# Kernel optimization log

Measured on AMD Instinct MI355X. Metric: run time of the kernel, lower is better.

## Reference

```python
import jax, jax.numpy as jnp
import numpy as np

K = 16          # knn_graph k
FPS_RATIO = 0.5 # fps ratio
BN_EPS = 1e-5


def knn_idx(p, k):
    # p: [B, N, 3] -> neighbor indices [B, N, k] (loop=True: self included)
    n2 = jnp.sum(p * p, axis=-1)                                  # [B, N]
    d = n2[:, :, None] + n2[:, None, :] - 2.0 * jnp.einsum('bnc,bmc->bnm', p, p)
    _, idx = jax.lax.top_k(-d, k)                                 # smallest distances
    return idx


def gather_nbrs(x, idx):
    # x: [B, N, C], idx: [B, N, k] -> [B, N, k, C]
    return jax.vmap(lambda xb, ib: xb[ib])(x, idx)


def bn_silu(y, g, be):
    # training-mode BatchNorm over all rows (flattened) + SiLU, per PyG MLP defaults
    C = y.shape[-1]
    yf = y.reshape(-1, C)
    mu = jnp.mean(yf, axis=0)
    var = jnp.mean((yf - mu) ** 2, axis=0)
    return jax.nn.silu((y - mu) * jax.lax.rsqrt(var + BN_EPS) * g + be)


def fps_idx(p, m):
    # farthest point sampling on one cloud p: [N, 3], deterministic start at 0
    d0 = jnp.sum((p - p[0]) ** 2, axis=-1)
    def step(mind, _):
        i = jnp.argmax(mind)
        di = jnp.sum((p - p[i]) ** 2, axis=-1)
        return jnp.minimum(mind, di), i.astype(jnp.int32)
    _, idxs = jax.lax.scan(step, d0, None, length=m - 1)
    return jnp.concatenate([jnp.zeros((1,), jnp.int32), idxs])


def setup_inputs() -> dict:
    key = jax.random.key(0)
    ks = jax.random.split(key, 4)
    B, N, zdim = 16, 2048, 256
    return {
        'pos': jax.random.normal(ks[0], (B, N, 3), jnp.float32),
        'W1': jax.random.normal(ks[1], (6, 64), jnp.float32) * (1.0 / np.sqrt(6)),
        'b1': jnp.zeros((64,), jnp.float32),
        'g1': jnp.ones((64,), jnp.float32),
        'be1': jnp.zeros((64,), jnp.float32),
        'W2a': jax.random.normal(ks[2], (67, 128), jnp.float32) * (1.0 / np.sqrt(67)),
        'b2a': jnp.zeros((128,), jnp.float32),
        'g2a': jnp.ones((128,), jnp.float32),
        'be2a': jnp.zeros((128,), jnp.float32),
        'W2b': jax.random.normal(ks[3], (128, zdim), jnp.float32) * (1.0 / np.sqrt(128)),
        'b2b': jnp.zeros((zdim,), jnp.float32),
        'g2b': jnp.ones((zdim,), jnp.float32),
        'be2b': jnp.zeros((zdim,), jnp.float32),
    }


def reference(pos, W1, b1, g1, be1, W2a, b2a, g2a, be2a, W2b, b2b, g2b, be2b):
    B, N, _ = pos.shape
    M = int(N * FPS_RATIO)

    # conv1: knn graph on pos, message = MLP([x_j, pos_j - pos_i]), max-aggr
    idx1 = knn_idx(pos, K)                                  # [B, N, K]
    pos_j = gather_nbrs(pos, idx1)                          # [B, N, K, 3]
    msg = jnp.concatenate([pos_j, pos_j - pos[:, :, None, :]], axis=-1)  # [B,N,K,6]
    h = bn_silu(msg @ W1 + b1, g1, be1)                     # [B, N, K, 64]
    h = jnp.max(h, axis=2)                                  # [B, N, 64]

    # farthest point sampling, ratio 0.5
    idx_f = jax.vmap(fps_idx, in_axes=(0, None))(pos, M)    # [B, M]
    h = jax.vmap(lambda a, i: a[i])(h, idx_f)               # [B, M, 64]
    pos2 = jax.vmap(lambda a, i: a[i])(pos, idx_f)          # [B, M, 3]

    # conv2: knn on sampled points, message = MLP2([h_j, pos_j - pos_i]), max-aggr
    idx2 = knn_idx(pos2, K)                                 # [B, M, K]
    h_j = gather_nbrs(h, idx2)                              # [B, M, K, 64]
    p_j = gather_nbrs(pos2, idx2)                           # [B, M, K, 3]
    msg2 = jnp.concatenate([h_j, p_j - pos2[:, :, None, :]], axis=-1)  # [B,M,K,67]
    h2 = bn_silu(msg2 @ W2a + b2a, g2a, be2a)               # [B, M, K, 128]
    h2 = bn_silu(h2 @ W2b + b2b, g2b, be2b)                 # [B, M, K, zdim]
    h2 = jnp.max(h2, axis=2)                                # [B, M, zdim]

    # global max aggregation per cloud
    return jnp.max(h2, axis=1)                              # [B, zdim]
```

## Files before the change

kernel.cpp:

```cpp
#include <hip/hip_runtime.h>
#include <hip/hip_bf16.h>

#define NB 16
#define NN 2048
#define KNNK 16
#define MM 1024
#define RC1 (NB*NN*KNNK)
#define RC2 (NB*MM*KNNK)

typedef unsigned long long u64;
typedef __attribute__((ext_vector_type(8))) short short8;
typedef __attribute__((ext_vector_type(4))) float f32x4;

__device__ __forceinline__ float frn_mul(float a, float b){ return __fmul_rn(a,b); }
__device__ __forceinline__ float frn_add(float a, float b){ return __fadd_rn(a,b); }
__device__ __forceinline__ float frn_sub(float a, float b){ return __fsub_rn(a,b); }
__device__ __forceinline__ float silu_f(float x){ return x / (1.0f + __expf(-x)); }
__device__ __forceinline__ u64 umax64(u64 a, u64 b){ return a > b ? a : b; }

__device__ __forceinline__ unsigned f32_sortable(float f){
  unsigned u = __float_as_uint(f);
  return u ^ ((unsigned)((int)u >> 31) | 0x80000000u);
}
__device__ __forceinline__ unsigned short f2bf(float f){
  unsigned u = __float_as_uint(f);
  return (unsigned short)((u + 0x7FFFu + ((u >> 16) & 1u)) >> 16);
}
__device__ __forceinline__ float bf2f(unsigned short h){
  return __uint_as_float(((unsigned)h) << 16);
}

__device__ __forceinline__ void atomicMaxF(unsigned* addr, float v){
  if (v >= 0.f) atomicMax((int*)addr, (int)__float_as_uint(v));
  else          atomicMin(addr, __float_as_uint(v));
}
__device__ __forceinline__ void atomicMinF(unsigned* addr, float v){
  if (v >= 0.f) atomicMin((int*)addr, (int)__float_as_uint(v));
  else          atomicMax(addr, __float_as_uint(v));
}

__global__ __launch_bounds__(256) void init_kernel(float* stats1, float* stats2a, float* stats2b,
                                                   unsigned* gmax, unsigned* gmin){
  int t = blockIdx.x*256 + threadIdx.x;
  if (t < 128) stats1[t] = 0.f;
  if (t < 256) stats2a[t] = 0.f;
  if (t < 512) stats2b[t] = 0.f;
  if (t < 4096){ gmax[t] = 0xFF800000u; gmin[t] = 0x7F800000u; }
}

template<int CHUNK>
__device__ __forceinline__ void knn_chunk_body(const float* __restrict__ pos_b, int qbase, int jbase,
                                               float4* sm, u64* __restrict__ out, int tid){
  for (int t = tid; t < CHUNK; t += 256){
    const float* p = pos_b + (size_t)(jbase + t)*3;
    float x = p[0], y = p[1], z = p[2];
    float n2 = frn_add(frn_add(frn_mul(x,x), frn_mul(y,y)), frn_mul(z,z));
    sm[t] = make_float4(x,y,z,n2);
  }
  __syncthreads();
  int i = qbase + tid;
  const float* qp = pos_b + (size_t)i*3;
  float xi = qp[0], yi = qp[1], zi = qp[2];
  float n2i = frn_add(frn_add(frn_mul(xi,xi), frn_mul(yi,yi)), frn_mul(zi,zi));
  u64 best[KNNK];
#pragma unroll
  for (int p = 0; p < KNNK; ++p) best[p] = ~0ull;
  for (int jj = 0; jj < CHUNK; ++jj){
    float4 v = sm[jj];
    float e = frn_add(frn_add(frn_mul(xi,v.x), frn_mul(yi,v.y)), frn_mul(zi,v.z));
    float d = frn_sub(frn_add(n2i, v.w), frn_mul(2.0f, e));
    u64 key = ((u64)f32_sortable(d) << 32) | (unsigned)(jbase + jj);
    if (key < best[KNNK-1]){
      u64 cur = key;
#pragma unroll
      for (int p = 0; p < KNNK; ++p){
        u64 mn = best[p] < cur ? best[p] : cur;
        u64 mx = best[p] < cur ? cur : best[p];
        best[p] = mn; cur = mx;
      }
    }
  }
#pragma unroll
  for (int p = 0; p < KNNK; ++p) out[p] = best[p];
}

__global__ __launch_bounds__(256) void k0_fps_knn1(const float* __restrict__ pos,
    int* __restrict__ idxf, float* __restrict__ pos2, u64* __restrict__ pknn1){
  __shared__ __align__(16) char smem[37*1024];
  int tid = threadIdx.x;
  if (blockIdx.x < 16){
    int b = blockIdx.x;
    float4* pts4 = (float4*)smem;
    int* sel = (int*)(smem + 32*1024);
    u64* wred = (u64*)(smem + 32*1024 + 4096);
    const float* pb = pos + (size_t)b*NN*3;
    float X[8], Y[8], Z[8], MD[8];
    unsigned LO[8];
#pragma unroll
    for (int q = 0; q < 8; ++q){
      int p = tid + 256*q;
      float x = pb[p*3+0], y = pb[p*3+1], z = pb[p*3+2];
      X[q] = x; Y[q] = y; Z[q] = z;
      LO[q] = ~(unsigned)p;
      pts4[p] = make_float4(x, y, z, 0.f);
    }
    float qx = pb[0], qy = pb[1], qz = pb[2];
#pragma unroll
    for (int q = 0; q < 8; ++q){
      float dx = frn_sub(X[q],qx), dy = frn_sub(Y[q],qy), dz = frn_sub(Z[q],qz);
      MD[q] = frn_add(frn_add(frn_mul(dx,dx), frn_mul(dy,dy)), frn_mul(dz,dz));
    }
    if (tid == 0) sel[0] = 0;
    int wv = tid >> 6;
    __syncthreads();
    for (int s = 1; s < MM; ++s){
      u64 t0 = umax64(((u64)__float_as_uint(MD[0])<<32)|LO[0], ((u64)__float_as_uint(MD[1])<<32)|LO[1]);
      u64 t1 = umax64(((u64)__float_as_uint(MD[2])<<32)|LO[2], ((u64)__float_as_uint(MD[3])<<32)|LO[3]);
      u64 t2 = umax64(((u64)__float_as_uint(MD[4])<<32)|LO[4], ((u64)__float_as_uint(MD[5])<<32)|LO[5]);
      u64 t3 = umax64(((u64)__float_as_uint(MD[6])<<32)|LO[6], ((u64)__float_as_uint(MD[7])<<32)|LO[7]);
      u64 kk = umax64(umax64(t0, t1), umax64(t2, t3));
#define RED_DPP(CTRL) { \
      unsigned lo_ = (unsigned)kk, hi_ = (unsigned)(kk>>32); \
      unsigned plo = (unsigned)__builtin_amdgcn_update_dpp((int)lo_,(int)lo_,CTRL,0xF,0xF,false); \
      unsigned phi = (unsigned)__builtin_amdgcn_update_dpp((int)hi_,(int)hi_,CTRL,0xF,0xF,false); \
      u64 o = ((u64)phi<<32)|plo; kk = o > kk ? o : kk; }
      RED_DPP(0xB1)
      RED_DPP(0x4E)
      RED_DPP(0x124)
      RED_DPP(0x128)
      RED_DPP(0x142)
      RED_DPP(0x143)
#undef RED_DPP
      int par = s & 1;
      if ((tid & 63) == 63) wred[par*4 + wv] = kk;
      __syncthreads();
      const u64* wr = wred + par*4;
      u64 K = umax64(umax64(wr[0], wr[1]), umax64(wr[2], wr[3]));
      unsigned wp = ~(unsigned)K;
      if (tid == 0) sel[s] = (int)wp;
      float4 wc = pts4[wp];
#pragma unroll
      for (int q = 0; q < 8; ++q){
        float dx = frn_sub(X[q],wc.x), dy = frn_sub(Y[q],wc.y), dz = frn_sub(Z[q],wc.z);
        float d = frn_add(frn_add(frn_mul(dx,dx), frn_mul(dy,dy)), frn_mul(dz,dz));
        MD[q] = fminf(MD[q], d);
      }
    }
    __syncthreads();
    for (int m = tid; m < MM; m += 256){
      int j = sel[m];
      idxf[b*MM + m] = j;
      float4 c = pts4[j];
      pos2[(size_t)(b*MM+m)*3+0] = c.x;
      pos2[(size_t)(b*MM+m)*3+1] = c.y;
      pos2[(size_t)(b*MM+m)*3+2] = c.z;
    }
  } else {
    int cid = blockIdx.x - 16;
    int b = cid >> 4;
    int rblk = (cid >> 1) & 7;
    int ch = cid & 1;
    float4* sm = (float4*)smem;
    const float* pos_b = pos + (size_t)b*NN*3;
    int i = rblk*256 + tid;
    u64* out = pknn1 + ((size_t)(b*NN + i)*2 + ch)*KNNK;
    knn_chunk_body<1024>(pos_b, rblk*256, ch*1024, sm, out, tid);
  }
}

__global__ __launch_bounds__(256) void k1_merge1_knn2(const u64* __restrict__ pknn1,
    int* __restrict__ idx1, const float* __restrict__ pos2, u64* __restrict__ pknn2){
  __shared__ __align__(16) float4 sm[256];
  int tid = threadIdx.x;
  if (blockIdx.x < 128){
    int row = blockIdx.x*256 + tid;
    const u64* A = pknn1 + (size_t)row*32;
    const u64* B = A + 16;
    int ia = 0, ib = 0;
    int* op = idx1 + (size_t)row*KNNK;
#pragma unroll
    for (int p = 0; p < KNNK; ++p){
      u64 ka = A[ia], kb = B[ib];
      if (ka < kb){ op[p] = (int)(unsigned)ka; ++ia; }
      else        { op[p] = (int)(unsigned)kb; ++ib; }
    }
  } else {
    int cid = blockIdx.x - 128;
    int b = cid >> 4;
    int rblk = (cid >> 2) & 3;
    int ch = cid & 3;
    const float* pos_b = pos2 + (size_t)b*MM*3;
    int i = rblk*256 + tid;
    u64* out = pknn2 + ((size_t)(b*MM + i)*4 + ch)*KNNK;
    knn_chunk_body<256>(pos_b, rblk*256, ch*256, sm, out, tid);
  }
}

__global__ __launch_bounds__(256) void k2_merge2_c1stats(const u64* __restrict__ pknn2,
    int* __restrict__ idx2, const float* __restrict__ pos, const int* __restrict__ idx1,
    const float* __restrict__ W1, const float* __restrict__ b1, float* __restrict__ stats1){
  __shared__ float red[4][64][2];
  int tid = threadIdx.x;
  if (blockIdx.x < 64){
    int row = blockIdx.x*256 + tid;
    const u64* L = pknn2 + (size_t)row*64;
    int o0=0, o1=0, o2=0, o3=0;
    int* op = idx2 + (size_t)row*KNNK;
#pragma unroll
    for (int p = 0; p < KNNK; ++p){
      u64 k0 = L[o0], k1 = L[16+o1], k2 = L[32+o2], k3 = L[48+o3];
      u64 m01 = k0 < k1 ? k0 : k1;
      u64 m23 = k2 < k3 ? k2 : k3;
      u64 m = m01 < m23 ? m01 : m23;
      op[p] = (int)(unsigned)m;
      o0 += (m == k0); o1 += (m == k1); o2 += (m == k2); o3 += (m == k3);
    }
    return;
  }
  int lane = tid & 63, wv = tid >> 6;
  int wave = (blockIdx.x - 64)*4 + wv;
  float w[6];
#pragma unroll
  for (int f = 0; f < 6; ++f) w[f] = W1[f*64 + lane];
  float bias = b1[lane];
  float ssum = 0.f, ssq = 0.f;
  for (int r = 0; r < 8; ++r){
    int row = wave*8 + r;
    int b = row >> 11, ii = row & 2047;
    const float* pi = pos + ((size_t)(b*NN + ii))*3;
    float xi = pi[0], yi = pi[1], zi = pi[2];
    const int* ip = idx1 + (size_t)row * KNNK;
#pragma unroll 4
    for (int k = 0; k < KNNK; ++k){
      int j = ip[k];
      const float* pj = pos + ((size_t)(b*NN + j))*3;
      float xj = pj[0], yj = pj[1], zj = pj[2];
      float y = bias;
      y = fmaf(xj, w[0], y); y = fmaf(yj, w[1], y); y = fmaf(zj, w[2], y);
      y = fmaf(xj - xi, w[3], y); y = fmaf(yj - yi, w[4], y); y = fmaf(zj - zi, w[5], y);
      ssum += y; ssq = fmaf(y, y, ssq);
    }
  }
  red[wv][lane][0] = ssum; red[wv][lane][1] = ssq;
  __syncthreads();
  if (tid < 64){
    float s = red[0][lane][0]+red[1][lane][0]+red[2][lane][0]+red[3][lane][0];
    float q = red[0][lane][1]+red[1][lane][1]+red[2][lane][1]+red[3][lane][1];
    atomicAdd(&stats1[lane], s);
    atomicAdd(&stats1[64+lane], q);
  }
}

__global__ __launch_bounds__(256) void conv1_apply_kernel(
    const float* __restrict__ pos, const int* __restrict__ idx1,
    const float* __restrict__ W1, const float* __restrict__ b1,
    const float* __restrict__ g1, const float* __restrict__ be1,
    const float* __restrict__ stats1, float* __restrict__ h){
  int lane = threadIdx.x & 63, wv = threadIdx.x >> 6;
  int wave = blockIdx.x*4 + wv;
  float w[6];
#pragma unroll
  for (int f = 0; f < 6; ++f) w[f] = W1[f*64 + lane];
  float bias = b1[lane];
  const float inv = 1.0f / (float)RC1;
  float mu = stats1[lane] * inv;
  float var = fmaxf(stats1[64+lane]*inv - mu*mu, 0.f);
  float sc = rsqrtf(var + 1e-5f) * g1[lane];
  float sh = be1[lane] - mu*sc;
  for (int r = 0; r < 8; ++r){
    int row = wave*8 + r;
    int b = row >> 11, ii = row & 2047;
    const float* pi = pos + ((size_t)(b*NN + ii))*3;
    float xi = pi[0], yi = pi[1], zi = pi[2];
    const int* ip = idx1 + (size_t)row * KNNK;
    float ymn = INFINITY, ymx = -INFINITY;
#pragma unroll 4
    for (int k = 0; k < KNNK; ++k){
      int j = ip[k];
      const float* pj = pos + ((size_t)(b*NN + j))*3;
      float xj = pj[0], yj = pj[1], zj = pj[2];
      float y = bias;
      y = fmaf(xj, w[0], y); y = fmaf(yj, w[1], y); y = fmaf(zj, w[2], y);
      y = fmaf(xj - xi, w[3], y); y = fmaf(yj - yi, w[4], y); y = fmaf(zj - zi, w[5], y);
      ymn = fminf(ymn, y); ymx = fmaxf(ymx, y);
    }
    h[((size_t)row << 6) + lane] = fmaxf(silu_f(fmaf(ymx, sc, sh)), silu_f(fmaf(ymn, sc, sh)));
  }
}

__global__ __launch_bounds__(256) void conv2a_kernel(
    const float* __restrict__ h, const int* __restrict__ idxf,
    const float* __restrict__ pos2, const int* __restrict__ idx2,
    const float* __restrict__ W2a, const float* __restrict__ b2a,
    float* __restrict__ stats2a, __hip_bfloat16* __restrict__ y2a){
  __shared__ float Wl[67*128];
  __shared__ float red[4][64][4];
  for (int t = threadIdx.x; t < 67*128; t += 256) Wl[t] = W2a[t];
  __syncthreads();
  int lane = threadIdx.x & 63, wv = threadIdx.x >> 6;
  int wave = blockIdx.x*4 + wv;
  float bias0 = b2a[lane], bias1 = b2a[64+lane];
  float ssum0=0, ssq0=0, ssum1=0, ssq1=0;
  for (int r4 = 0; r4 < 16; ++r4){
    int row0 = wave*64 + r4*4;
    int b = row0 >> 14;
    int m = (row0 >> 4) & 1023;
    int j0 = idx2[row0+0], j1 = idx2[row0+1], j2 = idx2[row0+2], j3 = idx2[row0+3];
    int q0 = idxf[b*MM + j0], q1 = idxf[b*MM + j1], q2 = idxf[b*MM + j2], q3 = idxf[b*MM + j3];
    const float4* h0 = (const float4*)(h + ((size_t)(b*NN + q0) << 6));
    const float4* h1 = (const float4*)(h + ((size_t)(b*NN + q1) << 6));
    const float4* h2 = (const float4*)(h + ((size_t)(b*NN + q2) << 6));
    const float4* h3 = (const float4*)(h + ((size_t)(b*NN + q3) << 6));
    float y00=bias0, y01=bias1, y10=bias0, y11=bias1;
    float y20=bias0, y21=bias1, y30=bias0, y31=bias1;
#define C2A_STEP(e, a0v, a1v, a2v, a3v) { \
      float w0_ = Wl[(e)*128 + lane], w1_ = Wl[(e)*128 + 64 + lane]; \
      y00 = fmaf(a0v, w0_, y00); y01 = fmaf(a0v, w1_, y01); \
      y10 = fmaf(a1v, w0_, y10); y11 = fmaf(a1v, w1_, y11); \
      y20 = fmaf(a2v, w0_, y20); y21 = fmaf(a2v, w1_, y21); \
      y30 = fmaf(a3v, w0_, y30); y31 = fmaf(a3v, w1_, y31); }
#pragma unroll
    for (int f4 = 0; f4 < 16; ++f4){
      float4 v0 = h0[f4], v1 = h1[f4], v2 = h2[f4], v3 = h3[f4];
      C2A_STEP(f4*4+0, v0.x, v1.x, v2.x, v3.x)
      C2A_STEP(f4*4+1, v0.y, v1.y, v2.y, v3.y)
      C2A_STEP(f4*4+2, v0.z, v1.z, v2.z, v3.z)
      C2A_STEP(f4*4+3, v0.w, v1.w, v2.w, v3.w)
    }
    const float* pm = pos2 + ((size_t)(b*MM + m))*3;
    float pmx = pm[0], pmy = pm[1], pmz = pm[2];
    const float* pj0 = pos2 + ((size_t)(b*MM + j0))*3;
    const float* pj1 = pos2 + ((size_t)(b*MM + j1))*3;
    const float* pj2 = pos2 + ((size_t)(b*MM + j2))*3;
    const float* pj3 = pos2 + ((size_t)(b*MM + j3))*3;
    C2A_STEP(64, pj0[0]-pmx, pj1[0]-pmx, pj2[0]-pmx, pj3[0]-pmx)
    C2A_STEP(65, pj0[1]-pmy, pj1[1]-pmy, pj2[1]-pmy, pj3[1]-pmy)
    C2A_STEP(66, pj0[2]-pmz, pj1[2]-pmz, pj2[2]-pmz, pj3[2]-pmz)
#undef C2A_STEP
    ssum0 += y00+y10+y20+y30;
    ssum1 += y01+y11+y21+y31;
    ssq0 = fmaf(y00,y00,fmaf(y10,y10,fmaf(y20,y20,fmaf(y30,y30,ssq0))));
    ssq1 = fmaf(y01,y01,fmaf(y11,y11,fmaf(y21,y21,fmaf(y31,y31,ssq1))));
    y2a[(size_t)(row0+0)*128 + lane]      = __float2bfloat16(y00);
    y2a[(size_t)(row0+0)*128 + 64 + lane] = __float2bfloat16(y01);
    y2a[(size_t)(row0+1)*128 + lane]      = __float2bfloat16(y10);
    y2a[(size_t)(row0+1)*128 + 64 + lane] = __float2bfloat16(y11);
    y2a[(size_t)(row0+2)*128 + lane]      = __float2bfloat16(y20);
    y2a[(size_t)(row0+2)*128 + 64 + lane] = __float2bfloat16(y21);
    y2a[(size_t)(row0+3)*128 + lane]      = __float2bfloat16(y30);
    y2a[(size_t)(row0+3)*128 + 64 + lane] = __float2bfloat16(y31);
  }
  red[wv][lane][0]=ssum0; red[wv][lane][1]=ssq0; red[wv][lane][2]=ssum1; red[wv][lane][3]=ssq1;
  __syncthreads();
  if (threadIdx.x < 64){
    float s0=0,q0=0,s1=0,q1=0;
#pragma unroll
    for (int v2=0; v2<4; ++v2){ s0+=red[v2][lane][0]; q0+=red[v2][lane][1]; s1+=red[v2][lane][2]; q1+=red[v2][lane][3]; }
    atomicAdd(&stats2a[lane], s0);      atomicAdd(&stats2a[128+lane], q0);
    atomicAdd(&stats2a[64+lane], s1);   atomicAdd(&stats2a[192+lane], q1);
  }
}

__global__ __launch_bounds__(256) void conv2b_kernel(
    const __hip_bfloat16* __restrict__ y2a, const float* __restrict__ stats2a,
    const float* __restrict__ g2a, const float* __restrict__ be2a,
    const float* __restrict__ W2b, const float* __restrict__ b2b,
    float* __restrict__ stats2b, unsigned* __restrict__ gmax, unsigned* __restrict__ gmin){
  __shared__ __align__(16) char Albs[64*256];
  __shared__ __align__(16) char Btbs[64*256];
  __shared__ float sc2a[128], sh2a[128];
  int tid = threadIdx.x;
  int lane = tid & 63, wvi = tid >> 6;
  int ct = blockIdx.x & 3;
  int rb = blockIdx.x >> 2;
  int c0 = ct * 64;
  int batch = rb >> 5;
  if (tid < 128){
    const float inv = 1.0f / (float)RC2;
    float mu = stats2a[tid] * inv;
    float var = fmaxf(stats2a[128+tid]*inv - mu*mu, 0.f);
    float s = rsqrtf(var + 1e-5f) * g2a[tid];
    sc2a[tid] = s; sh2a[tid] = be2a[tid] - mu*s;
  }
  {
    int cc = tid & 63, u0 = tid >> 6;
#pragma unroll
    for (int i = 0; i < 4; ++i){
      int u = u0 + i*4;
      unsigned short hb[8];
#pragma unroll
      for (int e = 0; e < 8; ++e) hb[e] = f2bf(W2b[(size_t)(u*8+e)*256 + c0 + cc]);
      *(short8*)(Btbs + cc*256 + u*16) = *(short8*)hb;
    }
  }
  __syncthreads();
  short8 bfrag[4];
#pragma unroll
  for (int kb4 = 0; kb4 < 4; ++kb4){
    int col_local = wvi*16 + (lane & 15);
    bfrag[kb4] = *(short8*)(Btbs + col_local*256 + kb4*64 + (lane>>4)*16);
  }
  float bb = b2b[c0 + wvi*16 + (lane & 15)];
  float vmn = INFINITY, vmx = -INFINITY, ssum = 0.f, ssq = 0.f;
  const unsigned short* y2u = (const unsigned short*)y2a;
  int sr = tid & 63, su = tid >> 6;
  for (int tile = 0; tile < 8; ++tile){
    int row0 = rb*512 + tile*64;
    if (tile > 0) __syncthreads();
#pragma unroll
    for (int i = 0; i < 4; ++i){
      int u = su + i*4;
      short8 v = *(const short8*)(y2u + (size_t)(row0 + sr)*128 + u*8);
      unsigned short ha[8];
#pragma unroll
      for (int e = 0; e < 8; ++e){
        int k = u*8 + e;
        float f = bf2f((unsigned short)v[e]);
        ha[e] = f2bf(silu_f(fmaf(f, sc2a[k], sh2a[k])));
      }
      *(short8*)(Albs + sr*256 + ((u*16) ^ ((sr & 7) << 4))) = *(short8*)ha;
    }
    __syncthreads();
#pragma unroll
    for (int sl = 0; sl < 4; ++sl){
      f32x4 acc = {0.f, 0.f, 0.f, 0.f};
#pragma unroll
      for (int kb4 = 0; kb4 < 4; ++kb4){
        int r = sl*16 + (lane & 15);
        short8 afrag = *(short8*)(Albs + r*256 + ((kb4*64 + (lane>>4)*16) ^ ((r & 7) << 4)));
        acc = __builtin_amdgcn_mfma_f32_16x16x32_bf16(afrag, bfrag[kb4], acc, 0, 0, 0);
      }
#pragma unroll
      for (int j = 0; j < 4; ++j){
        float y = acc[j] + bb;
        vmn = fminf(vmn, y); vmx = fmaxf(vmx, y);
        ssum += y; ssq = fmaf(y, y, ssq);
      }
    }
  }
#pragma unroll
  for (int off = 16; off <= 32; off += 16){
    vmn  = fminf(vmn,  __shfl_xor(vmn,  off));
    vmx  = fmaxf(vmx,  __shfl_xor(vmx,  off));
    ssum = ssum + __shfl_xor(ssum, off);
    ssq  = ssq  + __shfl_xor(ssq,  off);
  }
  if ((lane >> 4) == 0){
    int c = c0 + wvi*16 + lane;
    atomicAdd(&stats2b[c], ssum);
    atomicAdd(&stats2b[256+c], ssq);
    atomicMaxF(&gmax[batch*256 + c], vmx);
    atomicMinF(&gmin[batch*256 + c], vmn);
  }
}

__global__ __launch_bounds__(256) void final_kernel(
    const float* __restrict__ stats2b, const unsigned* __restrict__ gmax,
    const unsigned* __restrict__ gmin, const float* __restrict__ g2b,
    const float* __restrict__ be2b, float* __restrict__ out){
  int t = blockIdx.x*256 + threadIdx.x;
  if (t >= NB*256) return;
  int c = t & 255;
  const float inv = 1.0f / (float)RC2;
  float mu = stats2b[c]*inv;
  float var = fmaxf(stats2b[256+c]*inv - mu*mu, 0.f);
  float sc = rsqrtf(var + 1e-5f)*g2b[c];
  float sh = be2b[c] - mu*sc;
  float mx = __uint_as_float(gmax[t]);
  float mn = __uint_as_float(gmin[t]);
  out[t] = fmaxf(silu_f(fmaf(mx, sc, sh)), silu_f(fmaf(mn, sc, sh)));
}

extern "C" void kernel_launch(void* const* d_in, const int* in_sizes, int n_in,
                              void* d_out, int out_size, void* d_ws, size_t ws_size,
                              hipStream_t stream){
  (void)in_sizes; (void)n_in; (void)out_size; (void)ws_size;
  const float* pos  = (const float*)d_in[0];
  const float* W1   = (const float*)d_in[1];
  const float* b1   = (const float*)d_in[2];
  const float* g1   = (const float*)d_in[3];
  const float* be1  = (const float*)d_in[4];
  const float* W2a  = (const float*)d_in[5];
  const float* b2a  = (const float*)d_in[6];
  const float* g2a  = (const float*)d_in[7];
  const float* be2a = (const float*)d_in[8];
  const float* W2b  = (const float*)d_in[9];
  const float* b2b  = (const float*)d_in[10];
  const float* g2b  = (const float*)d_in[11];
  const float* be2b = (const float*)d_in[12];

  char* w = (char*)d_ws;
  size_t off = 0;
  auto carve = [&](size_t bytes)->void*{ void* p = w + off; off += (bytes + 255) & ~(size_t)255; return p; };
  int*      idx1    = (int*)carve((size_t)NB*NN*KNNK*4);
  float*    h       = (float*)carve((size_t)NB*NN*64*4);
  int*      idxf    = (int*)carve((size_t)NB*MM*4);
  float*    pos2    = (float*)carve((size_t)NB*MM*3*4);
  int*      idx2    = (int*)carve((size_t)NB*MM*KNNK*4);
  float*    stats1  = (float*)carve(128*4);
  float*    stats2a = (float*)carve(256*4);
  float*    stats2b = (float*)carve(512*4);
  unsigned* gmax    = (unsigned*)carve(4096*4);
  unsigned* gmin    = (unsigned*)carve(4096*4);
  __hip_bfloat16* y2a = (__hip_bfloat16*)carve((size_t)RC2*128*2);
  u64* pknn1 = (u64*)y2a;
  u64* pknn2 = (u64*)((char*)y2a + (32u<<20));

  init_kernel<<<dim3(16), dim3(256), 0, stream>>>(stats1, stats2a, stats2b, gmax, gmin);
  k0_fps_knn1<<<dim3(272), dim3(256), 0, stream>>>(pos, idxf, pos2, pknn1);
  k1_merge1_knn2<<<dim3(384), dim3(256), 0, stream>>>(pknn1, idx1, pos2, pknn2);
  k2_merge2_c1stats<<<dim3(1088), dim3(256), 0, stream>>>(pknn2, idx2, pos, idx1, W1, b1, stats1);
  conv1_apply_kernel<<<dim3(1024), dim3(256), 0, stream>>>(pos, idx1, W1, b1, g1, be1, stats1, h);
  conv2a_kernel<<<dim3(1024), dim3(256), 0, stream>>>(h, idxf, pos2, idx2, W2a, b2a, stats2a, y2a);
  conv2b_kernel<<<dim3(2048), dim3(256), 0, stream>>>(y2a, stats2a, g2a, be2a, W2b, b2b, stats2b, gmax, gmin);
  final_kernel<<<dim3(16), dim3(256), 0, stream>>>(stats2b, gmax, gmin, g2b, be2b, (float*)d_out);
}
```

Before: 970.3 us.

## Fuse knn1 with conv1 stats, drop partial-merge passes, merge knn2 with conv1 apply

Each knn1 block now scans all 2048 candidates itself instead of splitting the scan into two chunks, which removes the partial top-k buffers and the merge kernels. The neighbor indices are kept in shared memory and reused for the conv1 BatchNorm statistics in the same block. knn2 is computed without chunking inside the kernel that applies conv1. This cuts the launch count from seven to five and removes the intermediate global traffic, at the cost of fewer, longer knn blocks (128 instead of 256 for knn1, 64 instead of 256 for knn2), which lowers parallelism on a GPU with many CUs.

```diff
diff --git a/kernel.cpp b/kernel.cpp
--- a/kernel.cpp
+++ b/kernel.cpp
@@ -48,51 +48,16 @@
   if (t < 4096){ gmax[t] = 0xFF800000u; gmin[t] = 0x7F800000u; }
 }
 
-template<int CHUNK>
-__device__ __forceinline__ void knn_chunk_body(const float* __restrict__ pos_b, int qbase, int jbase,
-                                               float4* sm, u64* __restrict__ out, int tid){
-  for (int t = tid; t < CHUNK; t += 256){
-    const float* p = pos_b + (size_t)(jbase + t)*3;
-    float x = p[0], y = p[1], z = p[2];
-    float n2 = frn_add(frn_add(frn_mul(x,x), frn_mul(y,y)), frn_mul(z,z));
-    sm[t] = make_float4(x,y,z,n2);
-  }
-  __syncthreads();
-  int i = qbase + tid;
-  const float* qp = pos_b + (size_t)i*3;
-  float xi = qp[0], yi = qp[1], zi = qp[2];
-  float n2i = frn_add(frn_add(frn_mul(xi,xi), frn_mul(yi,yi)), frn_mul(zi,zi));
-  u64 best[KNNK];
-#pragma unroll
-  for (int p = 0; p < KNNK; ++p) best[p] = ~0ull;
-  for (int jj = 0; jj < CHUNK; ++jj){
-    float4 v = sm[jj];
-    float e = frn_add(frn_add(frn_mul(xi,v.x), frn_mul(yi,v.y)), frn_mul(zi,v.z));
-    float d = frn_sub(frn_add(n2i, v.w), frn_mul(2.0f, e));
-    u64 key = ((u64)f32_sortable(d) << 32) | (unsigned)(jbase + jj);
-    if (key < best[KNNK-1]){
-      u64 cur = key;
-#pragma unroll
-      for (int p = 0; p < KNNK; ++p){
-        u64 mn = best[p] < cur ? best[p] : cur;
-        u64 mx = best[p] < cur ? cur : best[p];
-        best[p] = mn; cur = mx;
-      }
-    }
-  }
-#pragma unroll
-  for (int p = 0; p < KNNK; ++p) out[p] = best[p];
-}
-
-__global__ __launch_bounds__(256) void k0_fps_knn1(const float* __restrict__ pos,
-    int* __restrict__ idxf, float* __restrict__ pos2, u64* __restrict__ pknn1){
-  __shared__ __align__(16) char smem[37*1024];
+__global__ __launch_bounds__(256) void k0_mega(const float* __restrict__ pos,
+    int* __restrict__ idxf, float* __restrict__ pos2, int* __restrict__ idx1,
+    const float* __restrict__ W1, const float* __restrict__ b1, float* __restrict__ stats1){
+  __shared__ __align__(16) char smem[51*1024];
   int tid = threadIdx.x;
   if (blockIdx.x < 16){
     int b = blockIdx.x;
     float4* pts4 = (float4*)smem;
     int* sel = (int*)(smem + 32*1024);
-    u64* wred = (u64*)(smem + 32*1024 + 4096);
+    u64* wred = (u64*)(smem + 36*1024);
     const float* pb = pos + (size_t)b*NN*3;
     float X[8], Y[8], Z[8], MD[8];
     unsigned LO[8];
@@ -157,134 +122,149 @@
     }
   } else {
     int cid = blockIdx.x - 16;
-    int b = cid >> 4;
-    int rblk = (cid >> 1) & 7;
-    int ch = cid & 1;
-    float4* sm = (float4*)smem;
-    const float* pos_b = pos + (size_t)b*NN*3;
+    int b = cid >> 3, rblk = cid & 7;
+    float4* pts4 = (float4*)smem;
+    int* idxl = (int*)(smem + 32*1024);
+    float* red = (float*)(smem + 48*1024);
+    const float* pb = pos + (size_t)b*NN*3;
+    for (int i = tid; i < NN; i += 256){
+      float x = pb[i*3+0], y = pb[i*3+1], z = pb[i*3+2];
+      float n2 = frn_add(frn_add(frn_mul(x,x), frn_mul(y,y)), frn_mul(z,z));
+      pts4[i] = make_float4(x, y, z, n2);
+    }
+    __syncthreads();
     int i = rblk*256 + tid;
-    u64* out = pknn1 + ((size_t)(b*NN + i)*2 + ch)*KNNK;
-    knn_chunk_body<1024>(pos_b, rblk*256, ch*1024, sm, out, tid);
-  }
-}
-
-__global__ __launch_bounds__(256) void k1_merge1_knn2(const u64* __restrict__ pknn1,
-    int* __restrict__ idx1, const float* __restrict__ pos2, u64* __restrict__ pknn2){
-  __shared__ __align__(16) float4 sm[256];
-  int tid = threadIdx.x;
-  if (blockIdx.x < 128){
-    int row = blockIdx.x*256 + tid;
-    const u64* A = pknn1 + (size_t)row*32;
-    const u64* B = A + 16;
-    int ia = 0, ib = 0;
-    int* op = idx1 + (size_t)row*KNNK;
+    float4 qv = pts4[i];
+    float xi = qv.x, yi = qv.y, zi = qv.z, n2i = qv.w;
+    u64 best[KNNK];
+#pragma unroll
+    for (int p = 0; p < KNNK; ++p) best[p] = ~0ull;
+    for (int jj = 0; jj < NN; ++jj){
+      float4 v = pts4[jj];
+      float e = frn_add(frn_add(frn_mul(xi,v.x), frn_mul(yi,v.y)), frn_mul(zi,v.z));
+      float d = frn_sub(frn_add(n2i, v.w), frn_mul(2.0f, e));
+      u64 key = ((u64)f32_sortable(d) << 32) | (unsigned)jj;
+      if (key < best[KNNK-1]){
+        u64 cur = key;
+#pragma unroll
+        for (int p = 0; p < KNNK; ++p){
+          u64 mn = best[p] < cur ? best[p] : cur;
+          u64 mx = best[p] < cur ? cur : best[p];
+          best[p] = mn; cur = mx;
+        }
+      }
+    }
+    int* op = idx1 + ((size_t)(b*NN + i))*KNNK;
 #pragma unroll
     for (int p = 0; p < KNNK; ++p){
-      u64 ka = A[ia], kb = B[ib];
-      if (ka < kb){ op[p] = (int)(unsigned)ka; ++ia; }
-      else        { op[p] = (int)(unsigned)kb; ++ib; }
-    }
-  } else {
-    int cid = blockIdx.x - 128;
-    int b = cid >> 4;
-    int rblk = (cid >> 2) & 3;
-    int ch = cid & 3;
-    const float* pos_b = pos2 + (size_t)b*MM*3;
-    int i = rblk*256 + tid;
-    u64* out = pknn2 + ((size_t)(b*MM + i)*4 + ch)*KNNK;
-    knn_chunk_body<256>(pos_b, rblk*256, ch*256, sm, out, tid);
-  }
-}
-
-__global__ __launch_bounds__(256) void k2_merge2_c1stats(const u64* __restrict__ pknn2,
-    int* __restrict__ idx2, const float* __restrict__ pos, const int* __restrict__ idx1,
-    const float* __restrict__ W1, const float* __restrict__ b1, float* __restrict__ stats1){
-  __shared__ float red[4][64][2];
-  int tid = threadIdx.x;
-  if (blockIdx.x < 64){
-    int row = blockIdx.x*256 + tid;
-    const u64* L = pknn2 + (size_t)row*64;
-    int o0=0, o1=0, o2=0, o3=0;
-    int* op = idx2 + (size_t)row*KNNK;
-#pragma unroll
-    for (int p = 0; p < KNNK; ++p){
-      u64 k0 = L[o0], k1 = L[16+o1], k2 = L[32+o2], k3 = L[48+o3];
-      u64 m01 = k0 < k1 ? k0 : k1;
-      u64 m23 = k2 < k3 ? k2 : k3;
-      u64 m = m01 < m23 ? m01 : m23;
-      op[p] = (int)(unsigned)m;
-      o0 += (m == k0); o1 += (m == k1); o2 += (m == k2); o3 += (m == k3);
-    }
-    return;
-  }
-  int lane = tid & 63, wv = tid >> 6;
-  int wave = (blockIdx.x - 64)*4 + wv;
-  float w[6];
-#pragma unroll
-  for (int f = 0; f < 6; ++f) w[f] = W1[f*64 + lane];
-  float bias = b1[lane];
-  float ssum = 0.f, ssq = 0.f;
-  for (int r = 0; r < 8; ++r){
-    int row = wave*8 + r;
-    int b = row >> 11, ii = row & 2047;
-    const float* pi = pos + ((size_t)(b*NN + ii))*3;
-    float xi = pi[0], yi = pi[1], zi = pi[2];
-    const int* ip = idx1 + (size_t)row * KNNK;
+      int j = (int)(unsigned)(best[p] & 0xFFFFFFFFull);
+      op[p] = j;
+      idxl[tid*KNNK + p] = j;
+    }
+    __syncthreads();
+    int lane = tid & 63, wv = tid >> 6;
+    float w[6];
+#pragma unroll
+    for (int f = 0; f < 6; ++f) w[f] = W1[f*64 + lane];
+    float bias = b1[lane];
+    float ssum = 0.f, ssq = 0.f;
+    for (int r = 0; r < 64; ++r){
+      int lrow = wv*64 + r;
+      float4 pi = pts4[rblk*256 + lrow];
+      const int* ip = idxl + lrow*KNNK;
 #pragma unroll 4
-    for (int k = 0; k < KNNK; ++k){
-      int j = ip[k];
-      const float* pj = pos + ((size_t)(b*NN + j))*3;
-      float xj = pj[0], yj = pj[1], zj = pj[2];
-      float y = bias;
-      y = fmaf(xj, w[0], y); y = fmaf(yj, w[1], y); y = fmaf(zj, w[2], y);
-      y = fmaf(xj - xi, w[3], y); y = fmaf(yj - yi, w[4], y); y = fmaf(zj - zi, w[5], y);
-      ssum += y; ssq = fmaf(y, y, ssq);
-    }
-  }
-  red[wv][lane][0] = ssum; red[wv][lane][1] = ssq;
-  __syncthreads();
-  if (tid < 64){
-    float s = red[0][lane][0]+red[1][lane][0]+red[2][lane][0]+red[3][lane][0];
-    float q = red[0][lane][1]+red[1][lane][1]+red[2][lane][1]+red[3][lane][1];
-    atomicAdd(&stats1[lane], s);
-    atomicAdd(&stats1[64+lane], q);
-  }
-}
-
-__global__ __launch_bounds__(256) void conv1_apply_kernel(
+      for (int k = 0; k < KNNK; ++k){
+        int j = ip[k];
+        float4 pj = pts4[j];
+        float y = bias;
+        y = fmaf(pj.x, w[0], y); y = fmaf(pj.y, w[1], y); y = fmaf(pj.z, w[2], y);
+        y = fmaf(pj.x - pi.x, w[3], y); y = fmaf(pj.y - pi.y, w[4], y); y = fmaf(pj.z - pi.z, w[5], y);
+        ssum += y; ssq = fmaf(y, y, ssq);
+      }
+    }
+    red[(wv*64+lane)*2+0] = ssum; red[(wv*64+lane)*2+1] = ssq;
+    __syncthreads();
+    if (tid < 64){
+      float s = red[(0*64+lane)*2]+red[(1*64+lane)*2]+red[(2*64+lane)*2]+red[(3*64+lane)*2];
+      float q = red[(0*64+lane)*2+1]+red[(1*64+lane)*2+1]+red[(2*64+lane)*2+1]+red[(3*64+lane)*2+1];
+      atomicAdd(&stats1[lane], s);
+      atomicAdd(&stats1[64+lane], q);
+    }
+  }
+}
+
+__global__ __launch_bounds__(256) void k1_knn2_c1apply(
+    const float* __restrict__ pos2, int* __restrict__ idx2,
     const float* __restrict__ pos, const int* __restrict__ idx1,
     const float* __restrict__ W1, const float* __restrict__ b1,
     const float* __restrict__ g1, const float* __restrict__ be1,
     const float* __restrict__ stats1, float* __restrict__ h){
-  int lane = threadIdx.x & 63, wv = threadIdx.x >> 6;
-  int wave = blockIdx.x*4 + wv;
-  float w[6];
-#pragma unroll
-  for (int f = 0; f < 6; ++f) w[f] = W1[f*64 + lane];
-  float bias = b1[lane];
-  const float inv = 1.0f / (float)RC1;
-  float mu = stats1[lane] * inv;
-  float var = fmaxf(stats1[64+lane]*inv - mu*mu, 0.f);
-  float sc = rsqrtf(var + 1e-5f) * g1[lane];
-  float sh = be1[lane] - mu*sc;
-  for (int r = 0; r < 8; ++r){
-    int row = wave*8 + r;
-    int b = row >> 11, ii = row & 2047;
-    const float* pi = pos + ((size_t)(b*NN + ii))*3;
-    float xi = pi[0], yi = pi[1], zi = pi[2];
-    const int* ip = idx1 + (size_t)row * KNNK;
-    float ymn = INFINITY, ymx = -INFINITY;
+  __shared__ __align__(16) float4 sm[1024];
+  int tid = threadIdx.x;
+  if (blockIdx.x < 64){
+    int b = blockIdx.x >> 2, rblk = blockIdx.x & 3;
+    const float* pb = pos2 + (size_t)b*MM*3;
+    for (int t = tid; t < MM; t += 256){
+      float x = pb[t*3+0], y = pb[t*3+1], z = pb[t*3+2];
+      float n2 = frn_add(frn_add(frn_mul(x,x), frn_mul(y,y)), frn_mul(z,z));
+      sm[t] = make_float4(x, y, z, n2);
+    }
+    __syncthreads();
+    int i = rblk*256 + tid;
+    float4 qv = sm[i];
+    float xi = qv.x, yi = qv.y, zi = qv.z, n2i = qv.w;
+    u64 best[KNNK];
+#pragma unroll
+    for (int p = 0; p < KNNK; ++p) best[p] = ~0ull;
+    for (int jj = 0; jj < MM; ++jj){
+      float4 v = sm[jj];
+      float e = frn_add(frn_add(frn_mul(xi,v.x), frn_mul(yi,v.y)), frn_mul(zi,v.z));
+      float d = frn_sub(frn_add(n2i, v.w), frn_mul(2.0f, e));
+      u64 key = ((u64)f32_sortable(d) << 32) | (unsigned)jj;
+      if (key < best[KNNK-1]){
+        u64 cur = key;
+#pragma unroll
+        for (int p = 0; p < KNNK; ++p){
+          u64 mn = best[p] < cur ? best[p] : cur;
+          u64 mx = best[p] < cur ? cur : best[p];
+          best[p] = mn; cur = mx;
+        }
+      }
+    }
+    int* op = idx2 + ((size_t)(b*MM + i))*KNNK;
+#pragma unroll
+    for (int p = 0; p < KNNK; ++p) op[p] = (int)(unsigned)(best[p] & 0xFFFFFFFFull);
+  } else {
+    int lane = tid & 63, wv = tid >> 6;
+    int wave = (blockIdx.x - 64)*4 + wv;
+    float w[6];
+#pragma unroll
+    for (int f = 0; f < 6; ++f) w[f] = W1[f*64 + lane];
+    float bias = b1[lane];
+    const float inv = 1.0f / (float)RC1;
+    float mu = stats1[lane] * inv;
+    float var = fmaxf(stats1[64+lane]*inv - mu*mu, 0.f);
+    float sc = rsqrtf(var + 1e-5f) * g1[lane];
+    float sh = be1[lane] - mu*sc;
+    for (int r = 0; r < 8; ++r){
+      int row = wave*8 + r;
+      int b = row >> 11, ii = row & 2047;
+      const float* pi = pos + ((size_t)(b*NN + ii))*3;
+      float xi = pi[0], yi = pi[1], zi = pi[2];
+      const int* ip = idx1 + (size_t)row * KNNK;
+      float ymn = INFINITY, ymx = -INFINITY;
 #pragma unroll 4
-    for (int k = 0; k < KNNK; ++k){
-      int j = ip[k];
-      const float* pj = pos + ((size_t)(b*NN + j))*3;
-      float xj = pj[0], yj = pj[1], zj = pj[2];
-      float y = bias;
-      y = fmaf(xj, w[0], y); y = fmaf(yj, w[1], y); y = fmaf(zj, w[2], y);
-      y = fmaf(xj - xi, w[3], y); y = fmaf(yj - yi, w[4], y); y = fmaf(zj - zi, w[5], y);
-      ymn = fminf(ymn, y); ymx = fmaxf(ymx, y);
-    }
-    h[((size_t)row << 6) + lane] = fmaxf(silu_f(fmaf(ymx, sc, sh)), silu_f(fmaf(ymn, sc, sh)));
+      for (int k = 0; k < KNNK; ++k){
+        int j = ip[k];
+        const float* pj = pos + ((size_t)(b*NN + j))*3;
+        float xj = pj[0], yj = pj[1], zj = pj[2];
+        float y = bias;
+        y = fmaf(xj, w[0], y); y = fmaf(yj, w[1], y); y = fmaf(zj, w[2], y);
+        y = fmaf(xj - xi, w[3], y); y = fmaf(yj - yi, w[4], y); y = fmaf(zj - zi, w[5], y);
+        ymn = fminf(ymn, y); ymx = fmaxf(ymx, y);
+      }
+      h[((size_t)row << 6) + lane] = fmaxf(silu_f(fmaf(ymx, sc, sh)), silu_f(fmaf(ymn, sc, sh)));
+    }
   }
 }
 
@@ -503,14 +483,10 @@
   unsigned* gmax    = (unsigned*)carve(4096*4);
   unsigned* gmin    = (unsigned*)carve(4096*4);
   __hip_bfloat16* y2a = (__hip_bfloat16*)carve((size_t)RC2*128*2);
-  u64* pknn1 = (u64*)y2a;
-  u64* pknn2 = (u64*)((char*)y2a + (32u<<20));
 
   init_kernel<<<dim3(16), dim3(256), 0, stream>>>(stats1, stats2a, stats2b, gmax, gmin);
-  k0_fps_knn1<<<dim3(272), dim3(256), 0, stream>>>(pos, idxf, pos2, pknn1);
-  k1_merge1_knn2<<<dim3(384), dim3(256), 0, stream>>>(pknn1, idx1, pos2, pknn2);
-  k2_merge2_c1stats<<<dim3(1088), dim3(256), 0, stream>>>(pknn2, idx2, pos, idx1, W1, b1, stats1);
-  conv1_apply_kernel<<<dim3(1024), dim3(256), 0, stream>>>(pos, idx1, W1, b1, g1, be1, stats1, h);
+  k0_mega<<<dim3(144), dim3(256), 0, stream>>>(pos, idxf, pos2, idx1, W1, b1, stats1);
+  k1_knn2_c1apply<<<dim3(1088), dim3(256), 0, stream>>>(pos2, idx2, pos, idx1, W1, b1, g1, be1, stats1, h);
   conv2a_kernel<<<dim3(1024), dim3(256), 0, stream>>>(h, idxf, pos2, idx2, W2a, b2a, stats2a, y2a);
   conv2b_kernel<<<dim3(2048), dim3(256), 0, stream>>>(y2a, stats2a, g2a, be2a, W2b, b2b, stats2b, gmax, gmin);
   final_kernel<<<dim3(16), dim3(256), 0, stream>>>(stats2b, gmax, gmin, g2b, be2b, (float*)d_out);
```

After: 1.742 ms. 1.8x slower.

## Process two FPS clouds per block and interleave weight pairs in conv2a LDS

Applied to the files above, without the earlier changes.

The farthest-point-sampling part now has each block handle two point clouds together, so each serial iteration's reductions, barrier and LDS lookups are shared and the two clouds' independent work interleaves to hide latency. This halves the FPS block count and the number of serial barrier chains, but doubles register and LDS use per block. Point coordinates move from float4 to separate x/y/z arrays in LDS. Separately, conv2a stores its weights interleaved so each lane fetches its two output-channel weights with one float2 LDS load instead of two scalar loads.

```diff
diff --git a/kernel.cpp b/kernel.cpp
--- a/kernel.cpp
+++ b/kernel.cpp
@@ -86,77 +86,106 @@
 
 __global__ __launch_bounds__(256) void k0_fps_knn1(const float* __restrict__ pos,
     int* __restrict__ idxf, float* __restrict__ pos2, u64* __restrict__ pknn1){
-  __shared__ __align__(16) char smem[37*1024];
+  __shared__ __align__(16) char smem[57*1024];
   int tid = threadIdx.x;
-  if (blockIdx.x < 16){
-    int b = blockIdx.x;
-    float4* pts4 = (float4*)smem;
-    int* sel = (int*)(smem + 32*1024);
-    u64* wred = (u64*)(smem + 32*1024 + 4096);
-    const float* pb = pos + (size_t)b*NN*3;
-    float X[8], Y[8], Z[8], MD[8];
+  if (blockIdx.x < 8){
+    int b0 = blockIdx.x*2, b1 = b0 + 1;
+    float* pxA = (float*)smem;
+    float* pyA = pxA + 2048;
+    float* pzA = pyA + 2048;
+    float* pxB = pzA + 2048;
+    float* pyB = pxB + 2048;
+    float* pzB = pyB + 2048;
+    int* selA = (int*)(smem + 48*1024);
+    int* selB = selA + 1024;
+    u64* wredA = (u64*)(smem + 56*1024);
+    u64* wredB = wredA + 8;
+    const float* pbA = pos + (size_t)b0*NN*3;
+    const float* pbB = pos + (size_t)b1*NN*3;
+    float XA[8], YA[8], ZA[8], MDA[8];
+    float XB[8], YB[8], ZB[8], MDB[8];
     unsigned LO[8];
 #pragma unroll
     for (int q = 0; q < 8; ++q){
       int p = tid + 256*q;
-      float x = pb[p*3+0], y = pb[p*3+1], z = pb[p*3+2];
-      X[q] = x; Y[q] = y; Z[q] = z;
+      float xa = pbA[p*3+0], ya = pbA[p*3+1], za = pbA[p*3+2];
+      float xb = pbB[p*3+0], yb = pbB[p*3+1], zb = pbB[p*3+2];
+      XA[q]=xa; YA[q]=ya; ZA[q]=za;
+      XB[q]=xb; YB[q]=yb; ZB[q]=zb;
       LO[q] = ~(unsigned)p;
-      pts4[p] = make_float4(x, y, z, 0.f);
-    }
-    float qx = pb[0], qy = pb[1], qz = pb[2];
+      pxA[p]=xa; pyA[p]=ya; pzA[p]=za;
+      pxB[p]=xb; pyB[p]=yb; pzB[p]=zb;
+    }
+    float qxA = pbA[0], qyA = pbA[1], qzA = pbA[2];
+    float qxB = pbB[0], qyB = pbB[1], qzB = pbB[2];
 #pragma unroll
     for (int q = 0; q < 8; ++q){
-      float dx = frn_sub(X[q],qx), dy = frn_sub(Y[q],qy), dz = frn_sub(Z[q],qz);
-      MD[q] = frn_add(frn_add(frn_mul(dx,dx), frn_mul(dy,dy)), frn_mul(dz,dz));
-    }
-    if (tid == 0) sel[0] = 0;
+      float dxa = frn_sub(XA[q],qxA), dya = frn_sub(YA[q],qyA), dza = frn_sub(ZA[q],qzA);
+      MDA[q] = frn_add(frn_add(frn_mul(dxa,dxa), frn_mul(dya,dya)), frn_mul(dza,dza));
+      float dxb = frn_sub(XB[q],qxB), dyb = frn_sub(YB[q],qyB), dzb = frn_sub(ZB[q],qzB);
+      MDB[q] = frn_add(frn_add(frn_mul(dxb,dxb), frn_mul(dyb,dyb)), frn_mul(dzb,dzb));
+    }
+    if (tid == 0){ selA[0] = 0; selB[0] = 0; }
     int wv = tid >> 6;
     __syncthreads();
-    for (int s = 1; s < MM; ++s){
-      u64 t0 = umax64(((u64)__float_as_uint(MD[0])<<32)|LO[0], ((u64)__float_as_uint(MD[1])<<32)|LO[1]);
-      u64 t1 = umax64(((u64)__float_as_uint(MD[2])<<32)|LO[2], ((u64)__float_as_uint(MD[3])<<32)|LO[3]);
-      u64 t2 = umax64(((u64)__float_as_uint(MD[4])<<32)|LO[4], ((u64)__float_as_uint(MD[5])<<32)|LO[5]);
-      u64 t3 = umax64(((u64)__float_as_uint(MD[6])<<32)|LO[6], ((u64)__float_as_uint(MD[7])<<32)|LO[7]);
-      u64 kk = umax64(umax64(t0, t1), umax64(t2, t3));
-#define RED_DPP(CTRL) { \
+#define TREE8(MD) ( umax64( umax64( \
+      umax64(((u64)__float_as_uint(MD[0])<<32)|LO[0], ((u64)__float_as_uint(MD[1])<<32)|LO[1]), \
+      umax64(((u64)__float_as_uint(MD[2])<<32)|LO[2], ((u64)__float_as_uint(MD[3])<<32)|LO[3])), umax64( \
+      umax64(((u64)__float_as_uint(MD[4])<<32)|LO[4], ((u64)__float_as_uint(MD[5])<<32)|LO[5]), \
+      umax64(((u64)__float_as_uint(MD[6])<<32)|LO[6], ((u64)__float_as_uint(MD[7])<<32)|LO[7])) ) )
+#define RED_DPP(kk, CTRL) { \
       unsigned lo_ = (unsigned)kk, hi_ = (unsigned)(kk>>32); \
       unsigned plo = (unsigned)__builtin_amdgcn_update_dpp((int)lo_,(int)lo_,CTRL,0xF,0xF,false); \
       unsigned phi = (unsigned)__builtin_amdgcn_update_dpp((int)hi_,(int)hi_,CTRL,0xF,0xF,false); \
       u64 o = ((u64)phi<<32)|plo; kk = o > kk ? o : kk; }
-      RED_DPP(0xB1)
-      RED_DPP(0x4E)
-      RED_DPP(0x124)
-      RED_DPP(0x128)
-      RED_DPP(0x142)
-      RED_DPP(0x143)
+    for (int s = 1; s < MM; ++s){
+      u64 kkA = TREE8(MDA);
+      u64 kkB = TREE8(MDB);
+      RED_DPP(kkA, 0xB1)  RED_DPP(kkB, 0xB1)
+      RED_DPP(kkA, 0x4E)  RED_DPP(kkB, 0x4E)
+      RED_DPP(kkA, 0x124) RED_DPP(kkB, 0x124)
+      RED_DPP(kkA, 0x128) RED_DPP(kkB, 0x128)
+      RED_DPP(kkA, 0x142) RED_DPP(kkB, 0x142)
+      RED_DPP(kkA, 0x143) RED_DPP(kkB, 0x143)
+      int par = s & 1;
+      if ((tid & 63) == 63){ wredA[par*4 + wv] = kkA; wredB[par*4 + wv] = kkB; }
+      __syncthreads();
+      const u64* wrA = wredA + par*4;
+      const u64* wrB = wredB + par*4;
+      u64 KA = umax64(umax64(wrA[0], wrA[1]), umax64(wrA[2], wrA[3]));
+      u64 KB = umax64(umax64(wrB[0], wrB[1]), umax64(wrB[2], wrB[3]));
+      unsigned wpA = ~(unsigned)KA;
+      unsigned wpB = ~(unsigned)KB;
+      float wxA = pxA[wpA], wyA = pyA[wpA], wzA = pzA[wpA];
+      float wxB = pxB[wpB], wyB = pyB[wpB], wzB = pzB[wpB];
+      if (tid == 0){ selA[s] = (int)wpA; selB[s] = (int)wpB; }
+#pragma unroll
+      for (int q = 0; q < 8; ++q){
+        float dxa = frn_sub(XA[q],wxA), dya = frn_sub(YA[q],wyA), dza = frn_sub(ZA[q],wzA);
+        float da = frn_add(frn_add(frn_mul(dxa,dxa), frn_mul(dya,dya)), frn_mul(dza,dza));
+        MDA[q] = fminf(MDA[q], da);
+        float dxb = frn_sub(XB[q],wxB), dyb = frn_sub(YB[q],wyB), dzb = frn_sub(ZB[q],wzB);
+        float db = frn_add(frn_add(frn_mul(dxb,dxb), frn_mul(dyb,dyb)), frn_mul(dzb,dzb));
+        MDB[q] = fminf(MDB[q], db);
+      }
+    }
 #undef RED_DPP
-      int par = s & 1;
-      if ((tid & 63) == 63) wred[par*4 + wv] = kk;
-      __syncthreads();
-      const u64* wr = wred + par*4;
-      u64 K = umax64(umax64(wr[0], wr[1]), umax64(wr[2], wr[3]));
-      unsigned wp = ~(unsigned)K;
-      if (tid == 0) sel[s] = (int)wp;
-      float4 wc = pts4[wp];
-#pragma unroll
-      for (int q = 0; q < 8; ++q){
-        float dx = frn_sub(X[q],wc.x), dy = frn_sub(Y[q],wc.y), dz = frn_sub(Z[q],wc.z);
-        float d = frn_add(frn_add(frn_mul(dx,dx), frn_mul(dy,dy)), frn_mul(dz,dz));
-        MD[q] = fminf(MD[q], d);
-      }
-    }
+#undef TREE8
     __syncthreads();
     for (int m = tid; m < MM; m += 256){
-      int j = sel[m];
-      idxf[b*MM + m] = j;
-      float4 c = pts4[j];
-      pos2[(size_t)(b*MM+m)*3+0] = c.x;
-      pos2[(size_t)(b*MM+m)*3+1] = c.y;
-      pos2[(size_t)(b*MM+m)*3+2] = c.z;
+      int jA = selA[m];
+      idxf[b0*MM + m] = jA;
+      pos2[(size_t)(b0*MM+m)*3+0] = pxA[jA];
+      pos2[(size_t)(b0*MM+m)*3+1] = pyA[jA];
+      pos2[(size_t)(b0*MM+m)*3+2] = pzA[jA];
+      int jB = selB[m];
+      idxf[b1*MM + m] = jB;
+      pos2[(size_t)(b1*MM+m)*3+0] = pxB[jB];
+      pos2[(size_t)(b1*MM+m)*3+1] = pyB[jB];
+      pos2[(size_t)(b1*MM+m)*3+2] = pzB[jB];
     }
   } else {
-    int cid = blockIdx.x - 16;
+    int cid = blockIdx.x - 8;
     int b = cid >> 4;
     int rblk = (cid >> 1) & 7;
     int ch = cid & 1;
@@ -293,9 +322,12 @@
     const float* __restrict__ pos2, const int* __restrict__ idx2,
     const float* __restrict__ W2a, const float* __restrict__ b2a,
     float* __restrict__ stats2a, __hip_bfloat16* __restrict__ y2a){
-  __shared__ float Wl[67*128];
+  __shared__ __align__(16) float Wl[67*128];
   __shared__ float red[4][64][4];
-  for (int t = threadIdx.x; t < 67*128; t += 256) Wl[t] = W2a[t];
+  for (int t = threadIdx.x; t < 67*128; t += 256){
+    int f = t >> 7, r = t & 127;
+    Wl[t] = W2a[f*128 + (r >> 1) + (r & 1)*64];
+  }
   __syncthreads();
   int lane = threadIdx.x & 63, wv = threadIdx.x >> 6;
   int wave = blockIdx.x*4 + wv;
@@ -314,7 +346,8 @@
     float y00=bias0, y01=bias1, y10=bias0, y11=bias1;
     float y20=bias0, y21=bias1, y30=bias0, y31=bias1;
 #define C2A_STEP(e, a0v, a1v, a2v, a3v) { \
-      float w0_ = Wl[(e)*128 + lane], w1_ = Wl[(e)*128 + 64 + lane]; \
+      float2 wp2 = *(const float2*)&Wl[(e)*128 + lane*2]; \
+      float w0_ = wp2.x, w1_ = wp2.y; \
       y00 = fmaf(a0v, w0_, y00); y01 = fmaf(a0v, w1_, y01); \
       y10 = fmaf(a1v, w0_, y10); y11 = fmaf(a1v, w1_, y11); \
       y20 = fmaf(a2v, w0_, y20); y21 = fmaf(a2v, w1_, y21); \
@@ -507,7 +540,7 @@
   u64* pknn2 = (u64*)((char*)y2a + (32u<<20));
 
   init_kernel<<<dim3(16), dim3(256), 0, stream>>>(stats1, stats2a, stats2b, gmax, gmin);
-  k0_fps_knn1<<<dim3(272), dim3(256), 0, stream>>>(pos, idxf, pos2, pknn1);
+  k0_fps_knn1<<<dim3(264), dim3(256), 0, stream>>>(pos, idxf, pos2, pknn1);
   k1_merge1_knn2<<<dim3(384), dim3(256), 0, stream>>>(pknn1, idx1, pos2, pknn2);
   k2_merge2_c1stats<<<dim3(1088), dim3(256), 0, stream>>>(pknn2, idx2, pos, idx1, W1, b1, stats1);
   conv1_apply_kernel<<<dim3(1024), dim3(256), 0, stream>>>(pos, idx1, W1, b1, g1, be1, stats1, h);
```

Measured after the change: 1.255 ms. 29.3% more time.
